# Performance work log

Hardware: AMD Instinct MI355X
Metric: run time of the kernel (lower is better)

The kernel has to match this reference:

```python
import jax, jax.numpy as jnp
import numpy as np

DIM = 512
N_HEADS = 8
N_KV_HEADS = 4
HEAD_DIM = DIM // N_HEADS  # 64
N_REP = N_HEADS // N_KV_HEADS  # 2
THETA = 10000.0
EPS_RMS = 1e-6
EPS_Z = 1e-6


def setup_inputs() -> dict:
    key = jax.random.key(0)
    ks = jax.random.split(key, 6)
    s = 1.0 / np.sqrt(DIM)
    return {
        "x": jax.random.normal(ks[0], (4, 8192, DIM), dtype=jnp.float32),
        "norm_w": jnp.ones((DIM,), dtype=jnp.float32),
        "wq": jax.random.normal(ks[1], (DIM, DIM), dtype=jnp.float32) * s,
        "wk": jax.random.normal(ks[2], (N_KV_HEADS * HEAD_DIM, DIM), dtype=jnp.float32) * s,
        "wv": jax.random.normal(ks[3], (N_KV_HEADS * HEAD_DIM, DIM), dtype=jnp.float32) * s,
        "wo": jax.random.normal(ks[4], (DIM, DIM), dtype=jnp.float32) * s,
    }


def _rope_cos_sin(seq_len, head_dim):
    # freqs_cis = polar(1, t * theta^(-2i/d))
    inv = 1.0 / (THETA ** (jnp.arange(0, head_dim, 2, dtype=jnp.float32) / head_dim))
    ang = jnp.arange(seq_len, dtype=jnp.float32)[:, None] * inv[None, :]  # (S, d/2)
    return jnp.cos(ang), jnp.sin(ang)


def _apply_rope(t, cos, sin):
    # t: (B, S, H, d); complex rotation on consecutive pairs
    B, S, H, d = t.shape
    tr = t.reshape(B, S, H, d // 2, 2)
    xr, xi = tr[..., 0], tr[..., 1]
    c = cos[None, :, None, :]  # (1, S, 1, d/2)
    s = sin[None, :, None, :]
    out = jnp.stack([xr * c - xi * s, xr * s + xi * c], axis=-1)
    return out.reshape(B, S, H, d)


def _forward(x, norm_w, wq, wk, wv, wo):
    B, S, _ = x.shape
    # RMSNorm
    x = x * jax.lax.rsqrt(jnp.mean(x * x, axis=-1, keepdims=True) + EPS_RMS) * norm_w
    xq = (x @ wq.T).reshape(B, S, N_HEADS, HEAD_DIM)
    xk = (x @ wk.T).reshape(B, S, N_KV_HEADS, HEAD_DIM)
    xv = (x @ wv.T).reshape(B, S, N_KV_HEADS, HEAD_DIM)
    cos, sin = _rope_cos_sin(S, HEAD_DIM)
    xq = _apply_rope(xq, cos, sin)
    xk = _apply_rope(xk, cos, sin)
    # repeat_kv: (B,S,Hkv,d) -> (B,S,Hkv*n_rep,d)
    keys = jnp.repeat(xk, N_REP, axis=2)
    values = jnp.repeat(xv, N_REP, axis=2)
    # to (B, H, S, d)
    Q = jnp.transpose(xq, (0, 2, 1, 3))
    K = jnp.transpose(keys, (0, 2, 1, 3))
    V = jnp.transpose(values, (0, 2, 1, 3))
    phi = lambda t: jax.nn.elu(t) + 1.0
    Q_lin, K_lin = phi(Q), phi(K)
    # Faithful to source: elementwise product reduced over s -> (B,H,d)
    KV = jnp.einsum('bhsd,bhsd->bhd', K_lin, V)
    K_sum = K_lin.sum(axis=2)  # (B,H,d)
    Z = jnp.einsum('bhsd,bhd->bhs', Q_lin, K_sum)[..., None]  # (B,H,S,1)
    Y = Q_lin * KV[:, :, None, :] / (Z + EPS_Z)  # (B,H,S,d)
    Y = jnp.transpose(Y, (0, 2, 1, 3)).reshape(B, S, N_HEADS * HEAD_DIM)
    return Y @ wo.T


def reference(x, norm_w, wq, wk, wv, wo):
    return _forward(x, norm_w, wq, wk, wv, wo)
```

## Files before the change

### kernel.cpp

```cpp
#include <hip/hip_runtime.h>
#include <cmath>

typedef __attribute__((ext_vector_type(8))) short short8;
typedef __attribute__((ext_vector_type(4))) float floatx4;

#define T_TOK 32768
#define DIMK 512

__device__ __forceinline__ unsigned short f2bf(float f) {
  union { float f; unsigned int u; } v; v.f = f;
  unsigned int r = (v.u + 0x7fffu + ((v.u >> 16) & 1u)) >> 16;
  return (unsigned short)r;
}
__device__ __forceinline__ float bf2f(unsigned short h) {
  union { unsigned int u; float f; } v; v.u = ((unsigned int)h) << 16;
  return v.f;
}

__device__ __forceinline__ void gload_lds16(const unsigned short* g, unsigned short* ldsbase) {
  __builtin_amdgcn_global_load_lds(
      (const __attribute__((address_space(1))) unsigned int*)g,
      (__attribute__((address_space(3))) unsigned int*)ldsbase, 16, 0, 0);
}

__global__ __launch_bounds__(256) void k_prep(const float* __restrict__ x,
    const float* __restrict__ norm_w, const float* __restrict__ wq,
    const float* __restrict__ wk, const float* __restrict__ wv,
    const float* __restrict__ wo, unsigned short* __restrict__ Wb,
    unsigned short* __restrict__ wob, float2* __restrict__ rope,
    float* __restrict__ KVz, unsigned short* __restrict__ xn) {
  if (blockIdx.x < 2048) {
    int i = blockIdx.x * 256 + threadIdx.x;
    float v;
    if (i < 262144) v = wq[i];
    else if (i < 393216) v = wk[i - 262144];
    else v = wv[i - 393216];
    Wb[i] = f2bf(v);
    if (i < 262144) {
      wob[i] = f2bf(wo[i]);
      int s = i >> 5, m = i & 31;
      const double c0 = 0.74989420933245582;
      double c1 = c0 * c0, c2 = c1 * c1, c3 = c2 * c2, c4 = c3 * c3;
      double p = 1.0;
      if (m & 1)  p *= c0;
      if (m & 2)  p *= c1;
      if (m & 4)  p *= c2;
      if (m & 8)  p *= c3;
      if (m & 16) p *= c4;
      double ang = (double)s * p;
      const double TWO_PI = 6.2831853071795864769;
      double q = rint(ang * (1.0 / TWO_PI));
      double r = fma(-q, TWO_PI, ang);
      float rf = (float)r;
      rope[i] = make_float2(cosf(rf), sinf(rf));
    }
    if (i < 2048) KVz[i] = 0.f;
  } else {
    int bid = blockIdx.x - 2048;
    int wave = threadIdx.x >> 6, lane = threadIdx.x & 63;
    size_t t = (size_t)bid * 4 + wave;
    const float4* xr = (const float4*)(x + t * DIMK);
    float4 a = xr[lane * 2];
    float4 b = xr[lane * 2 + 1];
    float ss = a.x * a.x + a.y * a.y + a.z * a.z + a.w * a.w
             + b.x * b.x + b.y * b.y + b.z * b.z + b.w * b.w;
    #pragma unroll
    for (int off = 32; off >= 1; off >>= 1) ss += __shfl_xor(ss, off, 64);
    float scale = rsqrtf(ss * (1.0f / DIMK) + 1e-6f);
    const float4* wr = (const float4*)norm_w;
    float4 w0 = wr[lane * 2], w1 = wr[lane * 2 + 1];
    uint4 o;
    o.x = (unsigned int)f2bf(a.x * scale * w0.x) | ((unsigned int)f2bf(a.y * scale * w0.y) << 16);
    o.y = (unsigned int)f2bf(a.z * scale * w0.z) | ((unsigned int)f2bf(a.w * scale * w0.w) << 16);
    o.z = (unsigned int)f2bf(b.x * scale * w1.x) | ((unsigned int)f2bf(b.y * scale * w1.y) << 16);
    o.w = (unsigned int)f2bf(b.z * scale * w1.z) | ((unsigned int)f2bf(b.w * scale * w1.w) << 16);
    *(uint4*)(xn + t * DIMK + lane * 8) = o;
  }
}

template <bool BF16_OUT>
__global__ __launch_bounds__(256) void k_gemm128(const unsigned short* __restrict__ A,
    const unsigned short* __restrict__ Bw, void* __restrict__ Cv, int N) {
  constexpr int K = DIMK;
  constexpr int BK = 64;
  __shared__ __align__(16) unsigned short As[128 * BK];
  __shared__ __align__(16) unsigned short Bs[128 * BK];
  const int tid = threadIdx.x;
  const int wave = tid >> 6, lane = tid & 63;
  const int r = lane & 15, quad = lane >> 4;
  const int wm = (wave >> 1) * 64, wn = (wave & 1) * 64;
  const int m0 = blockIdx.x * 128, n0 = blockIdx.y * 128;

  const int srow = (lane >> 3);
  const int scol = (((lane & 7) ^ srow)) * 8;
  const unsigned short* Ag[4];
  const unsigned short* Bg[4];
  unsigned short* Al[4];
  unsigned short* Bl[4];
  #pragma unroll
  for (int li = 0; li < 4; li++) {
    int row = wave * 32 + li * 8 + srow;
    Ag[li] = A  + (size_t)(m0 + row) * K + scol;
    Bg[li] = Bw + (size_t)(n0 + row) * K + scol;
    Al[li] = &As[(wave * 4 + li) * 512];
    Bl[li] = &Bs[(wave * 4 + li) * 512];
  }

  floatx4 acc[4][4];
  #pragma unroll
  for (int i = 0; i < 4; i++)
    #pragma unroll
    for (int j = 0; j < 4; j++)
      acc[i][j] = (floatx4){0.f, 0.f, 0.f, 0.f};

  const int r7 = r & 7;
  for (int k0 = 0; k0 < K; k0 += BK) {
    #pragma unroll
    for (int li = 0; li < 4; li++) {
      gload_lds16(Ag[li] + k0, Al[li]);
      gload_lds16(Bg[li] + k0, Bl[li]);
    }
    __syncthreads();
    #pragma unroll
    for (int kk = 0; kk < BK; kk += 32) {
      const int sw = ((((kk >> 3) + quad) ^ r7)) * 8;
      short8 af[4], bfv[4];
      #pragma unroll
      for (int i = 0; i < 4; i++)
        af[i] = *(const short8*)&As[(wm + i * 16 + r) * BK + sw];
      #pragma unroll
      for (int j = 0; j < 4; j++)
        bfv[j] = *(const short8*)&Bs[(wn + j * 16 + r) * BK + sw];
      #pragma unroll
      for (int i = 0; i < 4; i++)
        #pragma unroll
        for (int j = 0; j < 4; j++)
          acc[i][j] = __builtin_amdgcn_mfma_f32_16x16x32_bf16(af[i], bfv[j], acc[i][j], 0, 0, 0);
    }
    __syncthreads();
  }
  #pragma unroll
  for (int i = 0; i < 4; i++)
    #pragma unroll
    for (int j = 0; j < 4; j++) {
      int row = m0 + wm + i * 16 + quad * 4;
      int col = n0 + wn + j * 16 + r;
      #pragma unroll
      for (int p = 0; p < 4; p++) {
        if constexpr (BF16_OUT) {
          ((unsigned short*)Cv)[(size_t)(row + p) * N + col] = f2bf(acc[i][j][p]);
        } else {
          ((float*)Cv)[(size_t)(row + p) * N + col] = acc[i][j][p];
        }
      }
    }
}

__global__ __launch_bounds__(256) void k_kvred(const unsigned short* __restrict__ qkv,
    const float2* __restrict__ rope, float* __restrict__ KV, float* __restrict__ Ksum) {
  int bk = blockIdx.y;
  int b = bk >> 2, kh = bk & 3;
  int tid = threadIdx.x;
  int m = tid & 31;
  int sl = tid >> 5;
  int s0 = blockIdx.x * 256;
  float kvr = 0.f, kvi = 0.f, ksr = 0.f, ksi = 0.f;
  for (int si = sl; si < 256; si += 8) {
    int s = s0 + si;
    size_t t = (size_t)b * 8192 + s;
    const unsigned short* base = qkv + t * 1024;
    unsigned int kp = *(const unsigned int*)(base + 512 + kh * 64 + 2 * m);
    unsigned int vp = *(const unsigned int*)(base + 768 + kh * 64 + 2 * m);
    float kx = bf2f((unsigned short)(kp & 0xffffu));
    float ky = bf2f((unsigned short)(kp >> 16));
    float vx = bf2f((unsigned short)(vp & 0xffffu));
    float vy = bf2f((unsigned short)(vp >> 16));
    float2 cs = rope[s * 32 + m];
    float kr = kx * cs.x - ky * cs.y;
    float ki = kx * cs.y + ky * cs.x;
    kr = kr > 0.f ? kr + 1.f : __expf(kr);
    ki = ki > 0.f ? ki + 1.f : __expf(ki);
    kvr += kr * vx; kvi += ki * vy;
    ksr += kr;      ksi += ki;
  }
  __shared__ float red[256 * 4];
  red[tid * 4 + 0] = kvr; red[tid * 4 + 1] = kvi;
  red[tid * 4 + 2] = ksr; red[tid * 4 + 3] = ksi;
  __syncthreads();
  if (sl == 0) {
    for (int q = 1; q < 8; q++) {
      kvr += red[(q * 32 + m) * 4 + 0]; kvi += red[(q * 32 + m) * 4 + 1];
      ksr += red[(q * 32 + m) * 4 + 2]; ksi += red[(q * 32 + m) * 4 + 3];
    }
    atomicAdd(&KV[bk * 64 + 2 * m], kvr);
    atomicAdd(&KV[bk * 64 + 2 * m + 1], kvi);
    atomicAdd(&Ksum[bk * 64 + 2 * m], ksr);
    atomicAdd(&Ksum[bk * 64 + 2 * m + 1], ksi);
  }
}

__global__ __launch_bounds__(256) void k_qkern(const unsigned short* __restrict__ qkv,
    const float2* __restrict__ rope, const float* __restrict__ KV,
    const float* __restrict__ Ksum, unsigned short* __restrict__ Yb) {
  const int h = threadIdx.x >> 5;
  const int pr = threadIdx.x & 31;
  for (int t = blockIdx.x; t < T_TOK; t += gridDim.x) {
    int b = t >> 13, pos = t & 8191;
    unsigned int qp = *(const unsigned int*)(qkv + (size_t)t * 1024 + h * 64 + 2 * pr);
    float qx = bf2f((unsigned short)(qp & 0xffffu));
    float qy = bf2f((unsigned short)(qp >> 16));
    float2 cs = rope[pos * 32 + pr];
    float ar = qx * cs.x - qy * cs.y;
    float ai = qx * cs.y + qy * cs.x;
    ar = ar > 0.f ? ar + 1.f : __expf(ar);
    ai = ai > 0.f ? ai + 1.f : __expf(ai);
    int bk = b * 4 + (h >> 1);
    float2 ks = *(const float2*)(Ksum + bk * 64 + 2 * pr);
    float z = ar * ks.x + ai * ks.y;
    #pragma unroll
    for (int off = 16; off >= 1; off >>= 1) z += __shfl_xor(z, off, 64);
    float2 kv = *(const float2*)(KV + bk * 64 + 2 * pr);
    float inv = 1.0f / (z + 1e-6f);
    unsigned int o = (unsigned int)f2bf(ar * kv.x * inv)
                   | ((unsigned int)f2bf(ai * kv.y * inv) << 16);
    *(unsigned int*)(Yb + (size_t)t * 512 + h * 64 + 2 * pr) = o;
  }
}

extern "C" void kernel_launch(void* const* d_in, const int* in_sizes, int n_in,
                              void* d_out, int out_size, void* d_ws, size_t ws_size,
                              hipStream_t stream) {
  const float* x = (const float*)d_in[0];
  const float* norm_w = (const float*)d_in[1];
  const float* wq = (const float*)d_in[2];
  const float* wk = (const float*)d_in[3];
  const float* wv = (const float*)d_in[4];
  const float* wo = (const float*)d_in[5];
  float* out = (float*)d_out;

  char* ws = (char*)d_ws;
  unsigned short* xn  = (unsigned short*)(ws);
  unsigned short* Wb  = (unsigned short*)(ws + 33554432);
  unsigned short* wob = (unsigned short*)(ws + 34603008);
  unsigned short* qkv = (unsigned short*)(ws + 35127296);
  float2* rope        = (float2*)(ws + 102236160);
  float* KV           = (float*)(ws + 104333312);
  float* Ksum         = (float*)(ws + 104337408);
  unsigned short* Yb  = (unsigned short*)(ws + 104341504);

  k_prep<<<10240, 256, 0, stream>>>(x, norm_w, wq, wk, wv, wo, Wb, wob, rope, KV, xn);
  k_gemm128<true><<<dim3(256, 8), 256, 0, stream>>>(xn, Wb, (void*)qkv, 1024);
  k_kvred<<<dim3(32, 16), 256, 0, stream>>>(qkv, rope, KV, Ksum);
  k_qkern<<<4096, 256, 0, stream>>>(qkv, rope, KV, Ksum, Yb);
  k_gemm128<false><<<dim3(256, 4), 256, 0, stream>>>(Yb, wob, (void*)out, 512);
}
```

Before: 234.1 us.

## Replace 128x128 GEMM with double-buffered 256x256 tile, 8 waves, XCD-aware block remap

Both bf16 GEMMs now use 256x256 output tiles with 512 threads, 128KB dynamic LDS holding two K-stage buffers, and a hand-scheduled ping-pong of LDS reads, async global-to-LDS loads and MFMA quadrants with s_setprio and explicit vmcnt waits. Block IDs are remapped across the 8 XCDs to improve L2 locality. The goal is to hide global load latency behind MFMA work and raise data reuse per tile. In exchange, occupancy drops to one large workgroup per CU, there are many more barriers, and far fewer blocks are launched (512 and 256).

New measurement: 227.1 us. -3.0%, faster.

```diff
diff --git a/kernel.cpp b/kernel.cpp
--- a/kernel.cpp
+++ b/kernel.cpp
@@ -79,68 +79,114 @@
 }
 
 template <bool BF16_OUT>
-__global__ __launch_bounds__(256) void k_gemm128(const unsigned short* __restrict__ A,
+__global__ __launch_bounds__(512, 2) void k_gemm256(const unsigned short* __restrict__ A,
     const unsigned short* __restrict__ Bw, void* __restrict__ Cv, int N) {
   constexpr int K = DIMK;
-  constexpr int BK = 64;
-  __shared__ __align__(16) unsigned short As[128 * BK];
-  __shared__ __align__(16) unsigned short Bs[128 * BK];
+  extern __shared__ __align__(16) unsigned short smem[];
+  unsigned short* const AsP = smem;
+  unsigned short* const BsP = smem + 32768;
+
   const int tid = threadIdx.x;
   const int wave = tid >> 6, lane = tid & 63;
-  const int r = lane & 15, quad = lane >> 4;
-  const int wm = (wave >> 1) * 64, wn = (wave & 1) * 64;
-  const int m0 = blockIdx.x * 128, n0 = blockIdx.y * 128;
-
-  const int srow = (lane >> 3);
-  const int scol = (((lane & 7) ^ srow)) * 8;
-  const unsigned short* Ag[4];
-  const unsigned short* Bg[4];
-  unsigned short* Al[4];
-  unsigned short* Bl[4];
+  const int r = lane & 15, quad = lane >> 4, r7 = r & 7;
+  const int wm = (wave >> 2) * 128, wn = (wave & 3) * 64;
+
+  const int nwg = gridDim.x * gridDim.y;
+  const int bid = blockIdx.x + gridDim.x * blockIdx.y;
+  const int cpx = nwg >> 3;
+  const int nid = (bid & 7) * cpx + (bid >> 3);
+  const int m0 = (nid & 127) * 256;
+  const int n0 = (nid >> 7) * 256;
+
+  const int srow = lane >> 3;
+  const int scb = (lane & 7) ^ srow;
+  const unsigned short* const Asrc = A + (size_t)(m0 + wave * 8 + srow) * K + scb * 8;
+  const unsigned short* const Bsrc = Bw + (size_t)(n0 + wave * 8 + srow) * K + scb * 8;
+  unsigned short* const Adst = AsP + wave * 8 * 64;
+  unsigned short* const Bdst = BsP + wave * 8 * 64;
+
+#define STAGE_A(buf, h, kt) do { \
+    gload_lds16(Asrc + (size_t)((h) * 128) * K + (kt) * 64, Adst + (buf) * 16384 + ((h) * 128) * 64); \
+    gload_lds16(Asrc + (size_t)((h) * 128 + 64) * K + (kt) * 64, Adst + (buf) * 16384 + ((h) * 128 + 64) * 64); \
+  } while (0)
+#define STAGE_B(buf, h, kt) do { \
+    gload_lds16(Bsrc + (size_t)((h) * 128) * K + (kt) * 64, Bdst + (buf) * 16384 + ((h) * 128) * 64); \
+    gload_lds16(Bsrc + (size_t)((h) * 128 + 64) * K + (kt) * 64, Bdst + (buf) * 16384 + ((h) * 128 + 64) * 64); \
+  } while (0)
+
+  short8 af[4][2], b0[2][2], b1[2][2];
+  floatx4 acc[8][4];
   #pragma unroll
-  for (int li = 0; li < 4; li++) {
-    int row = wave * 32 + li * 8 + srow;
-    Ag[li] = A  + (size_t)(m0 + row) * K + scol;
-    Bg[li] = Bw + (size_t)(n0 + row) * K + scol;
-    Al[li] = &As[(wave * 4 + li) * 512];
-    Bl[li] = &Bs[(wave * 4 + li) * 512];
-  }
-
-  floatx4 acc[4][4];
-  #pragma unroll
-  for (int i = 0; i < 4; i++)
+  for (int i = 0; i < 8; i++)
     #pragma unroll
     for (int j = 0; j < 4; j++)
       acc[i][j] = (floatx4){0.f, 0.f, 0.f, 0.f};
 
-  const int r7 = r & 7;
-  for (int k0 = 0; k0 < K; k0 += BK) {
-    #pragma unroll
-    for (int li = 0; li < 4; li++) {
-      gload_lds16(Ag[li] + k0, Al[li]);
-      gload_lds16(Bg[li] + k0, Bl[li]);
-    }
-    __syncthreads();
-    #pragma unroll
-    for (int kk = 0; kk < BK; kk += 32) {
-      const int sw = ((((kk >> 3) + quad) ^ r7)) * 8;
-      short8 af[4], bfv[4];
-      #pragma unroll
-      for (int i = 0; i < 4; i++)
-        af[i] = *(const short8*)&As[(wm + i * 16 + r) * BK + sw];
-      #pragma unroll
-      for (int j = 0; j < 4; j++)
-        bfv[j] = *(const short8*)&Bs[(wn + j * 16 + r) * BK + sw];
-      #pragma unroll
-      for (int i = 0; i < 4; i++)
-        #pragma unroll
-        for (int j = 0; j < 4; j++)
-          acc[i][j] = __builtin_amdgcn_mfma_f32_16x16x32_bf16(af[i], bfv[j], acc[i][j], 0, 0, 0);
-    }
-    __syncthreads();
-  }
+#define LDA8(buf, ah) do { \
+    _Pragma("unroll") for (int ii = 0; ii < 4; ii++) \
+      _Pragma("unroll") for (int kk = 0; kk < 2; kk++) \
+        af[ii][kk] = *(const short8*)&AsP[(buf) * 16384 + (wm + (ah) * 64 + ii * 16 + r) * 64 + ((kk * 4 + quad) ^ r7) * 8]; \
+  } while (0)
+#define LDB4(buf, bh, arr) do { \
+    _Pragma("unroll") for (int jj = 0; jj < 2; jj++) \
+      _Pragma("unroll") for (int kk = 0; kk < 2; kk++) \
+        arr[jj][kk] = *(const short8*)&BsP[(buf) * 16384 + (wn + (bh) * 32 + jj * 16 + r) * 64 + ((kk * 4 + quad) ^ r7) * 8]; \
+  } while (0)
+#define MFMAQ(ah, bh, arr) do { \
+    __builtin_amdgcn_s_setprio(1); \
+    _Pragma("unroll") for (int ii = 0; ii < 4; ii++) \
+      _Pragma("unroll") for (int jj = 0; jj < 2; jj++) \
+        _Pragma("unroll") for (int kk = 0; kk < 2; kk++) \
+          acc[(ah) * 4 + ii][(bh) * 2 + jj] = __builtin_amdgcn_mfma_f32_16x16x32_bf16( \
+              af[ii][kk], arr[jj][kk], acc[(ah) * 4 + ii][(bh) * 2 + jj], 0, 0, 0); \
+    __builtin_amdgcn_s_setprio(0); \
+  } while (0)
+#define BAR() do { asm volatile("" ::: "memory"); __builtin_amdgcn_s_barrier(); asm volatile("" ::: "memory"); } while (0)
+#define VMW(n) do { asm volatile("s_waitcnt vmcnt(" #n ")" ::: "memory"); __builtin_amdgcn_sched_barrier(0); } while (0)
+
+  STAGE_A(0, 0, 0); STAGE_B(0, 0, 0); STAGE_A(0, 1, 0); STAGE_B(0, 1, 0);
+  STAGE_A(1, 0, 1); STAGE_B(1, 0, 1); STAGE_A(1, 1, 1); STAGE_B(1, 1, 1);
+  VMW(8);
+  BAR();
+
   #pragma unroll
-  for (int i = 0; i < 4; i++)
+  for (int it = 0; it < 3; ++it) {
+    const int kt = it * 2;
+    LDA8(0, 0); LDB4(0, 0, b0);
+    BAR(); MFMAQ(0, 0, b0); BAR();
+    LDB4(0, 1, b1);
+    BAR(); MFMAQ(0, 1, b1); BAR();
+    LDA8(0, 1); STAGE_B(0, 0, kt + 2); STAGE_B(0, 1, kt + 2);
+    BAR(); MFMAQ(1, 1, b1); BAR();
+    STAGE_A(0, 0, kt + 2); STAGE_A(0, 1, kt + 2);
+    BAR(); MFMAQ(1, 0, b0); VMW(8); BAR();
+    LDA8(1, 0); LDB4(1, 0, b0);
+    BAR(); MFMAQ(0, 0, b0); BAR();
+    LDB4(1, 1, b1);
+    BAR(); MFMAQ(0, 1, b1); BAR();
+    LDA8(1, 1); STAGE_B(1, 0, kt + 3); STAGE_B(1, 1, kt + 3);
+    BAR(); MFMAQ(1, 1, b1); BAR();
+    STAGE_A(1, 0, kt + 3); STAGE_A(1, 1, kt + 3);
+    BAR(); MFMAQ(1, 0, b0); VMW(8); BAR();
+  }
+
+  LDA8(0, 0); LDB4(0, 0, b0);
+  BAR(); MFMAQ(0, 0, b0); BAR();
+  LDB4(0, 1, b1);
+  BAR(); MFMAQ(0, 1, b1); BAR();
+  LDA8(0, 1);
+  BAR(); MFMAQ(1, 1, b1); BAR();
+  MFMAQ(1, 0, b0); VMW(0); BAR();
+  LDA8(1, 0); LDB4(1, 0, b0);
+  BAR(); MFMAQ(0, 0, b0); BAR();
+  LDB4(1, 1, b1);
+  BAR(); MFMAQ(0, 1, b1); BAR();
+  LDA8(1, 1);
+  BAR(); MFMAQ(1, 1, b1); BAR();
+  MFMAQ(1, 0, b0);
+
+  #pragma unroll
+  for (int i = 0; i < 8; i++)
     #pragma unroll
     for (int j = 0; j < 4; j++) {
       int row = m0 + wm + i * 16 + quad * 4;
@@ -154,6 +200,13 @@
         }
       }
     }
+#undef STAGE_A
+#undef STAGE_B
+#undef LDA8
+#undef LDB4
+#undef MFMAQ
+#undef BAR
+#undef VMW
 }
 
 __global__ __launch_bounds__(256) void k_kvred(const unsigned short* __restrict__ qkv,
@@ -248,9 +301,18 @@
   float* Ksum         = (float*)(ws + 104337408);
   unsigned short* Yb  = (unsigned short*)(ws + 104341504);
 
+  static bool s_attr = false;
+  if (!s_attr) {
+    (void)hipFuncSetAttribute(reinterpret_cast<const void*>(&k_gemm256<true>),
+                              hipFuncAttributeMaxDynamicSharedMemorySize, 131072);
+    (void)hipFuncSetAttribute(reinterpret_cast<const void*>(&k_gemm256<false>),
+                              hipFuncAttributeMaxDynamicSharedMemorySize, 131072);
+    s_attr = true;
+  }
+
   k_prep<<<10240, 256, 0, stream>>>(x, norm_w, wq, wk, wv, wo, Wb, wob, rope, KV, xn);
-  k_gemm128<true><<<dim3(256, 8), 256, 0, stream>>>(xn, Wb, (void*)qkv, 1024);
+  k_gemm256<true><<<dim3(128, 4), 512, 131072, stream>>>(xn, Wb, (void*)qkv, 1024);
   k_kvred<<<dim3(32, 16), 256, 0, stream>>>(qkv, rope, KV, Ksum);
   k_qkern<<<4096, 256, 0, stream>>>(qkv, rope, KV, Ksum, Yb);
-  k_gemm128<false><<<dim3(256, 4), 256, 0, stream>>>(Yb, wob, (void*)out, 512);
-}
+  k_gemm256<false><<<dim3(128, 2), 512, 131072, stream>>>(Yb, wob, (void*)out, 512);
+}
```
